# Optimization experiments

Measured on AMD Instinct MI355X. Metric: run time of the kernel, lower is better.

Reference implementation:

```python
import jax, jax.numpy as jnp
import numpy as np

M = 64    # multiplicity (channels per harmonic degree)
P = 64    # positional encoding dim
EPS = 1e-5


def sinusoidal_pe(N, P):
    pos = jnp.arange(N, dtype=jnp.float32)[:, None]
    div = jnp.exp(jnp.arange(0, P, 2, dtype=jnp.float32) * (-np.log(10000.0) / P))
    pe = jnp.zeros((N, P), dtype=jnp.float32)
    pe = pe.at[:, 0::2].set(jnp.sin(pos * div))
    pe = pe.at[:, 1::2].set(jnp.cos(pos * div))
    return pe


def split_irreps(h):
    # h: [B, N, 4M] -> scalar part [B,N,M], vector part [B,N,M,3]
    B, N, _ = h.shape
    h4 = h.reshape(B, N, M, 4)
    return h4[..., 0], h4[..., 1:]


def merge_irreps(s, v):
    B, N, _ = s.shape
    return jnp.concatenate([s[..., None], v], axis=-1).reshape(B, N, M * 4)


def hyena_block(h, Wq, Wk, Wv, filt, Wo):
    # Hyena-style gated long convolution: q * conv(k * v), FFT circular conv along seq
    N = h.shape[1]
    q = h @ Wq
    k = h @ Wk
    v = h @ Wv
    kf = jnp.fft.rfft(filt, n=N, axis=0)                       # [N//2+1, H]
    conv = jnp.fft.irfft(jnp.fft.rfft(k * v, n=N, axis=1) * kf[None], n=N, axis=1)
    return (q * conv) @ Wo


def reg_linear(h, W0, W1):
    # degree-wise linear mixing across multiplicity (equivariant)
    s, v = split_irreps(h)
    return merge_irreps(jnp.einsum('bnm,mk->bnk', s, W0),
                        jnp.einsum('bnmd,mk->bnkd', v, W1))


def reg_batchnorm(h, g0, g1):
    # normalize per-channel irrep norms over (batch, tokens); learnable per-channel gain
    s, v = split_irreps(h)
    n0 = jnp.sqrt(jnp.mean(s * s, axis=(0, 1)) + EPS)          # [M]
    n1 = jnp.sqrt(jnp.mean(jnp.sum(v * v, axis=-1), axis=(0, 1)) + EPS)
    return merge_irreps(s / n0 * g0, v / n1[:, None] * g1[:, None])


def norm_activation(h):
    # norm-gated nonlinearity: each irrep scaled by sigmoid of its norm (equivariant)
    s, v = split_irreps(h)
    vn = jnp.sqrt(jnp.sum(v * v, axis=-1, keepdims=True) + EPS)
    return merge_irreps(s * jax.nn.sigmoid(jnp.abs(s)), v * jax.nn.sigmoid(vn))


def setup_inputs() -> dict:
    key = jax.random.key(0)
    B, N = 64, 1024
    D = M * 4
    H = [360, 360, 160]   # 10*sum(2l+1,l<=5)=360, 360, 10*sum(2l+1,l<=3)=160
    ks = iter(jax.random.split(key, 64))
    def rn(shape, scale=0.02):
        return jax.random.normal(next(ks), shape, dtype=jnp.float32) * scale
    inp = {
        'x': jax.random.normal(next(ks), (B, N, 3), dtype=jnp.float32),
        'tok_emb': rn((3, P)),
        'Wf': rn((P, M)),
        'wv': rn((M,), 0.5),
        'w_out': rn((M,), 0.5),
    }
    for i, Hi in enumerate(H, start=1):
        inp[f'Wq{i}'] = rn((D, Hi)); inp[f'Wk{i}'] = rn((D, Hi)); inp[f'Wv{i}'] = rn((D, Hi))
        inp[f'filt{i}'] = rn((N, Hi)); inp[f'Wo{i}'] = rn((Hi, D))
        inp[f'Wm0_{i}'] = rn((M, M)); inp[f'Wm1_{i}'] = rn((M, M))
        inp[f'g0_{i}'] = jnp.ones((M,), jnp.float32); inp[f'g1_{i}'] = jnp.ones((M,), jnp.float32)
    return inp


def reference(x, tok_emb, Wf, wv, w_out,
              Wq1, Wk1, Wv1, filt1, Wo1, Wm0_1, Wm1_1, g0_1, g1_1,
              Wq2, Wk2, Wv2, filt2, Wo2, Wm0_2, Wm1_2, g0_2, g1_2,
              Wq3, Wk3, Wv3, filt3, Wo3, Wm0_3, Wm1_3, g0_3, g1_3):
    B, N, _ = x.shape
    # invariant features: sinusoidal PE + token-type embedding (alternating 0/1, last token 2)
    pe = sinusoidal_pe(N, P)
    tt = jnp.arange(N) % 2
    tt = tt.at[-1].set(2)
    f = pe + tok_emb[tt]                                        # [N, P]
    # input conversion: invariants -> degree-0 channels; input vector -> degree-1 channels
    s0 = jnp.broadcast_to((f @ Wf)[None], (B, N, M))
    v0 = x[:, :, None, :] * wv[None, None, :, None]             # [B, N, M, 3]
    h = merge_irreps(s0, v0)                                    # [B, N, 4M]
    layers = [
        (Wq1, Wk1, Wv1, filt1, Wo1, Wm0_1, Wm1_1, g0_1, g1_1),
        (Wq2, Wk2, Wv2, filt2, Wo2, Wm0_2, Wm1_2, g0_2, g1_2),
        (Wq3, Wk3, Wv3, filt3, Wo3, Wm0_3, Wm1_3, g0_3, g1_3),
    ]
    for (Wq, Wk, Wv_, filt, Wo, Wm0, Wm1, g0, g1) in layers:
        h = h + hyena_block(h, Wq, Wk, Wv_, filt, Wo)           # hyena + residual
        y = reg_linear(h, Wm0, Wm1)                             # mlp
        y = reg_batchnorm(y, g0, g1)                            # batch norm
        y = norm_activation(y)                                  # norm activation
        h = h + y                                               # residual
    pooled = h.mean(axis=1)                                     # [B, 4M] mean pool over tokens
    _, vpool = split_irreps(pooled[:, None, :])                 # [B, 1, M, 3]
    return jnp.einsum('bmd,m->bd', vpool[:, 0], w_out)          # [B, 3]
```

## Files before the change

### kernel.cpp

```cpp
#include <hip/hip_runtime.h>
#include <math.h>

namespace {

typedef __bf16 bf16_t;
typedef bf16_t bf16x8 __attribute__((ext_vector_type(8)));
typedef float floatx4 __attribute__((ext_vector_type(4)));

constexpr int kN = 1024;
constexpr int kM = 64;
constexpr int kP = 64;
constexpr float kEps = 1e-5f;
constexpr int kFN = 1024;
constexpr size_t kYOFF = 16777216;

__device__ __forceinline__ float sigmoidf(float v) { return 1.0f / (1.0f + expf(-v)); }

__device__ __forceinline__ floatx4 mfma16(bf16x8 a, bf16x8 b, floatx4 c) {
  return __builtin_amdgcn_mfma_f32_16x16x32_bf16(a, b, c, 0, 0, 0);
}

__device__ __forceinline__ void fma3(floatx4& acc, bf16x8 ah, bf16x8 al,
                                     bf16x8 bh, bf16x8 bl) {
  acc = mfma16(ah, bh, acc);
  acc = mfma16(ah, bl, acc);
  acc = mfma16(al, bh, acc);
}

__device__ __forceinline__ void fma2(floatx4& acc, bf16x8 ah, bf16x8 bh, bf16x8 bl) {
  acc = mfma16(ah, bh, acc);
  acc = mfma16(ah, bl, acc);
}

union U4 { uint4 u; bf16_t b[8]; };
union Pk4 { uint2 u; bf16_t b[4]; };
union Ub2 { uint u; bf16_t b[2]; };

__device__ __forceinline__ void glds16(const bf16_t* g, bf16_t* l) {
  __builtin_amdgcn_global_load_lds(
      (const __attribute__((address_space(1))) void*)g,
      (__attribute__((address_space(3))) void*)l, 16, 0, 0);
}

__device__ __forceinline__ size_t hidx(int r, int d8) {
  const int rb = r >> 6, rr = r & 63;
  return (size_t)(rb * 8 + (d8 >> 2)) * 4096 + (rr >> 4) * 1024 + (d8 & 3) * 128 + (rr & 15) * 8;
}

__device__ __forceinline__ int zi(int i) { return i + (i >> 4); }

__device__ __forceinline__ float2 cadd(float2 a, float2 b) { return {a.x + b.x, a.y + b.y}; }
__device__ __forceinline__ float2 csub(float2 a, float2 b) { return {a.x - b.x, a.y - b.y}; }
__device__ __forceinline__ float2 cmul(float2 a, float2 w) {
  return {a.x * w.x - a.y * w.y, a.x * w.y + a.y * w.x};
}
__device__ __forceinline__ float2 cmulc(float2 a, float2 w) {
  return {a.x * w.x + a.y * w.y, a.y * w.x - a.x * w.y};
}

__global__ void k_s0(const float* __restrict__ tok_emb, const float* __restrict__ Wf,
                     float* __restrict__ s0) {
  __shared__ float f[kP];
  const int n = blockIdx.x;
  const int t = threadIdx.x;
  const int tt = (n == kN - 1) ? 2 : (n & 1);
  const int j = t >> 1;
  const float cexp = (float)(-9.210340371976184 / 64.0);
  const float divj = expf((float)(2 * j) * cexp);
  const float ang = (float)n * divj;
  const float pe = (t & 1) ? cosf(ang) : sinf(ang);
  f[t] = pe + tok_emb[tt * kP + t];
  __syncthreads();
  float acc = 0.0f;
#pragma unroll 8
  for (int p = 0; p < kP; ++p) acc = fmaf(f[p], Wf[p * kM + t], acc);
  s0[n * kM + t] = acc;
}

__global__ void k_h0(const float* __restrict__ x, const float* __restrict__ wv,
                     const float* __restrict__ s0, bf16_t* __restrict__ hsh) {
  const int idx = blockIdx.x * 256 + threadIdx.x;
  const int r = idx >> 5, d8 = idx & 31;
  const int n = r & (kN - 1);
  const int m0 = d8 * 2, m1 = m0 + 1;
  const float w0 = wv[m0], w1 = wv[m1];
  const float x0 = x[r * 3 + 0], x1 = x[r * 3 + 1], x2 = x[r * 3 + 2];
  float f[8];
  f[0] = s0[n * kM + m0]; f[1] = x0 * w0; f[2] = x1 * w0; f[3] = x2 * w0;
  f[4] = s0[n * kM + m1]; f[5] = x0 * w1; f[6] = x1 * w1; f[7] = x2 * w1;
  U4 oh, ol;
#pragma unroll
  for (int i = 0; i < 8; ++i) {
    const bf16_t h_ = (bf16_t)f[i];
    oh.b[i] = h_; ol.b[i] = (bf16_t)(f[i] - (float)h_);
  }
  const size_t base = hidx(r, d8);
  *(uint4*)(hsh + base) = oh.u;
  *(uint4*)(hsh + base + 512) = ol.u;
}

__global__ void k_wqkv3(const float* __restrict__ Wq0, const float* __restrict__ Wk0,
                        const float* __restrict__ Wv0,
                        const float* __restrict__ Wq1, const float* __restrict__ Wk1,
                        const float* __restrict__ Wv1,
                        const float* __restrict__ Wq2, const float* __restrict__ Wk2,
                        const float* __restrict__ Wv2, bf16_t* __restrict__ wall3) {
  const int l = blockIdx.y;
  const int H = (l == 2) ? 160 : 360;
  const int gy = (l == 2) ? 3 : 6;
  const int c = blockIdx.x;
  if (c >= gy * 64) return;
  const int k = threadIdx.x;
  const float* Wq = (l == 0) ? Wq0 : ((l == 1) ? Wq1 : Wq2);
  const float* Wk = (l == 0) ? Wk0 : ((l == 1) ? Wk1 : Wk2);
  const float* Wv = (l == 0) ? Wv0 : ((l == 1) ? Wv1 : Wv2);
  bf16_t* wall = wall3 + ((l == 2) ? 1179648 : (size_t)l * 589824);
  const bool ok = c < H;
  const float w[3] = {ok ? Wq[k * H + c] : 0.f, ok ? Wk[k * H + c] : 0.f,
                      ok ? Wv[k * H + c] : 0.f};
  const int ct = c >> 6, cgrp = (c >> 4) & 3, cl = c & 15;
  const int kc = k >> 5, quad = (k >> 3) & 3, off = k & 7;
  const size_t base = (size_t)(ct * 8 + kc) * 12288 + cgrp * 512 + quad * 128 + cl * 8 + off;
#pragma unroll
  for (int mat = 0; mat < 3; ++mat) {
    const bf16_t hi = (bf16_t)w[mat];
    wall[base + mat * 4096] = hi;
    wall[base + mat * 4096 + 2048] = (bf16_t)(w[mat] - (float)hi);
  }
}

__global__ void k_wo3(const float* __restrict__ Wo0, const float* __restrict__ Wo1,
                      const float* __restrict__ Wo2, bf16_t* __restrict__ WoF3) {
  const int l = blockIdx.y;
  const int H = (l == 2) ? 160 : 360;
  const float* Wo = (l == 0) ? Wo0 : ((l == 1) ? Wo1 : Wo2);
  bf16_t* WoF = WoF3 + (size_t)l * 196608;
  const int d = blockIdx.x;
  const int c = threadIdx.x;
  const float w = (c < H) ? Wo[c * 256 + d] : 0.f;
  const int dt = d >> 6, dgrp = (d >> 4) & 3, dl = d & 15;
  const int kc = c >> 5, quad = (c >> 3) & 3, off = c & 7;
  const size_t base = (size_t)(dt * 12 + kc) * 4096 + dgrp * 512 + quad * 128 + dl * 8 + off;
  const bf16_t hi = (bf16_t)w;
  WoF[base] = hi;
  WoF[base + 2048] = (bf16_t)(w - (float)hi);
}

__global__ void k_bt3(const float* __restrict__ W00, const float* __restrict__ W10,
                      const float* __restrict__ W01, const float* __restrict__ W11,
                      const float* __restrict__ W02, const float* __restrict__ W12,
                      bf16_t* __restrict__ BtF3) {
  const int l = blockIdx.y;
  const float* W0 = (l == 0) ? W00 : ((l == 1) ? W01 : W02);
  const float* W1 = (l == 0) ? W10 : ((l == 1) ? W11 : W12);
  bf16_t* BtF = BtF3 + (size_t)l * 131072;
  const int col = blockIdx.x, row = threadIdx.x;
  const int k = col >> 2, ck = col & 3, m = row >> 2, cm = row & 3;
  float v = 0.f;
  if (cm == ck) v = (ck == 0 ? W0 : W1)[m * 64 + k];
  const int ct = col >> 6, cgrp = (col >> 4) & 3, cl = col & 15;
  const int kc = row >> 5, quad = (row >> 3) & 3, off = row & 7;
  const size_t base = (size_t)(ct * 8 + kc) * 4096 + cgrp * 512 + quad * 128 + cl * 8 + off;
  const bf16_t hi = (bf16_t)v;
  BtF[base] = hi;
  BtF[base + 2048] = (bf16_t)(v - (float)hi);
}

__global__ void k_tw(float2* __restrict__ twg) {
  const int j = blockIdx.x * 256 + threadIdx.x;
  if (j < kFN / 2) {
    float s, c;
    sincosf(-6.283185307179586f * (float)j / (float)kFN, &s, &c);
    twg[j].x = c; twg[j].y = s;
  }
}

__device__ __forceinline__ void dif_step(float2* z, const float2* tw, int m, int p) {
  const int pm = p & (m - 1);
  const int j = ((p & ~(m - 1)) << 2) | pm;
  const int tm2 = 512 / (2 * m), tm1 = 512 / m;
  const float2 x0 = z[zi(j)], x1 = z[zi(j + m)];
  const float2 x2 = z[zi(j + 2 * m)], x3 = z[zi(j + 3 * m)];
  const float2 w2 = tw[pm * tm2], w2b = tw[(pm + m) * tm2], w1 = tw[pm * tm1];
  const float2 a0 = cadd(x0, x2), a2 = cmul(csub(x0, x2), w2);
  const float2 a1 = cadd(x1, x3), a3 = cmul(csub(x1, x3), w2b);
  z[zi(j)]         = cadd(a0, a1);
  z[zi(j + m)]     = cmul(csub(a0, a1), w1);
  z[zi(j + 2 * m)] = cadd(a2, a3);
  z[zi(j + 3 * m)] = cmul(csub(a2, a3), w1);
}

__device__ __forceinline__ void dit_step(float2* z, const float2* tw, int m, int p) {
  const int pm = p & (m - 1);
  const int j = ((p & ~(m - 1)) << 2) | pm;
  const int tm2 = 512 / (2 * m), tm1 = 512 / m;
  const float2 x0 = z[zi(j)], x1 = z[zi(j + m)];
  const float2 x2 = z[zi(j + 2 * m)], x3 = z[zi(j + 3 * m)];
  const float2 w1 = tw[pm * tm1], w2 = tw[pm * tm2], w2b = tw[(pm + m) * tm2];
  const float2 c1 = cmulc(x1, w1), c3 = cmulc(x3, w1);
  const float2 b0 = cadd(x0, c1), b1 = csub(x0, c1);
  const float2 b2 = cadd(x2, c3), b3 = csub(x2, c3);
  const float2 d2 = cmulc(b2, w2), d3 = cmulc(b3, w2b);
  z[zi(j)]         = cadd(b0, d2);
  z[zi(j + 2 * m)] = csub(b0, d2);
  z[zi(j + m)]     = cadd(b1, d3);
  z[zi(j + 3 * m)] = csub(b1, d3);
}

__device__ void fft_dif(float2* z, const float2* tw) {
  const int p = threadIdx.x;
#pragma unroll
  for (int m = 256; m >= 1; m >>= 2) {
    __syncthreads();
    dif_step(z, tw, m, p);
  }
}

__device__ void fft_dif2(float2* za, float2* zb, const float2* tw) {
  const int p = threadIdx.x;
#pragma unroll
  for (int m = 256; m >= 1; m >>= 2) {
    __syncthreads();
    dif_step(za, tw, m, p);
    dif_step(zb, tw, m, p);
  }
}

__device__ void fft_dit_inv2(float2* za, float2* zb, const float2* tw) {
  const int p = threadIdx.x;
#pragma unroll
  for (int m = 1; m <= 256; m <<= 2) {
    __syncthreads();
    dit_step(za, tw, m, p);
    dit_step(zb, tw, m, p);
  }
}

__global__ __launch_bounds__(256) void k_kf3(const float* __restrict__ f0,
    const float* __restrict__ f1, const float* __restrict__ f2,
    const float2* __restrict__ twg, float2* __restrict__ kf3) {
  __shared__ float2 z[kFN + kFN / 16];
  __shared__ float2 tw[kFN / 2];
  const int bid = blockIdx.x;
  const int l = (bid < 360) ? 0 : ((bid < 720) ? 1 : 2);
  const int c = bid - ((l == 0) ? 0 : ((l == 1) ? 360 : 720));
  const int H = (l == 2) ? 160 : 360;
  const float* filt = (l == 0) ? f0 : ((l == 1) ? f1 : f2);
  float2* kf = kf3 + (size_t)l * 368640;
  for (int j = threadIdx.x; j < kFN / 2; j += 256) tw[j] = twg[j];
  for (int n = threadIdx.x; n < kFN; n += 256) {
    z[zi(n)].x = filt[n * H + c];
    z[zi(n)].y = 0.0f;
  }
  fft_dif(z, tw);
  __syncthreads();
  for (int j = threadIdx.x; j < kFN; j += 256) kf[c * kFN + j] = z[zi(j)];
}

__global__ __launch_bounds__(256) void k_conv(const bf16_t* __restrict__ kvb,
    const bf16_t* __restrict__ qb, bf16_t* __restrict__ prodb,
    const float2* __restrict__ kf, const float2* __restrict__ twg, int H) {
  __shared__ float2 za[kFN + kFN / 16];
  __shared__ float2 zb[kFN + kFN / 16];
  __shared__ float2 tw[kFN / 2];
  const int blk = blockIdx.x;
  const int c = blk % H;
  const int pb = blk / H;
  const size_t off0 = ((size_t)((4 * pb) * H + c)) << 10;
  const size_t off1 = ((size_t)((4 * pb + 1) * H + c)) << 10;
  const size_t off2 = ((size_t)((4 * pb + 2) * H + c)) << 10;
  const size_t off3 = ((size_t)((4 * pb + 3) * H + c)) << 10;
  for (int j = threadIdx.x; j < kFN / 2; j += 256) tw[j] = twg[j];
  for (int n2 = threadIdx.x; n2 < 512; n2 += 256) {
    Ub2 a0, a1, a2, a3;
    a0.u = *(const uint*)(kvb + off0 + 2 * n2);
    a1.u = *(const uint*)(kvb + off1 + 2 * n2);
    a2.u = *(const uint*)(kvb + off2 + 2 * n2);
    a3.u = *(const uint*)(kvb + off3 + 2 * n2);
    za[zi(2 * n2)].x = (float)a0.b[0];     za[zi(2 * n2)].y = (float)a1.b[0];
    za[zi(2 * n2 + 1)].x = (float)a0.b[1]; za[zi(2 * n2 + 1)].y = (float)a1.b[1];
    zb[zi(2 * n2)].x = (float)a2.b[0];     zb[zi(2 * n2)].y = (float)a3.b[0];
    zb[zi(2 * n2 + 1)].x = (float)a2.b[1]; zb[zi(2 * n2 + 1)].y = (float)a3.b[1];
  }
  fft_dif2(za, zb, tw);
  __syncthreads();
  for (int j = threadIdx.x; j < kFN; j += 256) {
    const float2 b = kf[c * kFN + j];
    const float2 a = za[zi(j)];
    float2 o;
    o.x = a.x * b.x - a.y * b.y;
    o.y = a.x * b.y + a.y * b.x;
    za[zi(j)] = o;
    const float2 a2_ = zb[zi(j)];
    float2 o2;
    o2.x = a2_.x * b.x - a2_.y * b.y;
    o2.y = a2_.x * b.y + a2_.y * b.x;
    zb[zi(j)] = o2;
  }
  fft_dit_inv2(za, zb, tw);
  __syncthreads();
  const float s = 1.0f / (float)kFN;
  for (int n2 = threadIdx.x; n2 < 512; n2 += 256) {
    Ub2 q0, q1, q2, q3, o0, o1, o2, o3;
    q0.u = *(const uint*)(qb + off0 + 2 * n2);
    q1.u = *(const uint*)(qb + off1 + 2 * n2);
    q2.u = *(const uint*)(qb + off2 + 2 * n2);
    q3.u = *(const uint*)(qb + off3 + 2 * n2);
    o0.b[0] = (bf16_t)((za[zi(2 * n2)].x * s) * (float)q0.b[0]);
    o0.b[1] = (bf16_t)((za[zi(2 * n2 + 1)].x * s) * (float)q0.b[1]);
    o1.b[0] = (bf16_t)((za[zi(2 * n2)].y * s) * (float)q1.b[0]);
    o1.b[1] = (bf16_t)((za[zi(2 * n2 + 1)].y * s) * (float)q1.b[1]);
    o2.b[0] = (bf16_t)((zb[zi(2 * n2)].x * s) * (float)q2.b[0]);
    o2.b[1] = (bf16_t)((zb[zi(2 * n2 + 1)].x * s) * (float)q2.b[1]);
    o3.b[0] = (bf16_t)((zb[zi(2 * n2)].y * s) * (float)q3.b[0]);
    o3.b[1] = (bf16_t)((zb[zi(2 * n2 + 1)].y * s) * (float)q3.b[1]);
    *(uint*)(prodb + off0 + 2 * n2) = o0.u;
    *(uint*)(prodb + off1 + 2 * n2) = o1.u;
    *(uint*)(prodb + off2 + 2 * n2) = o2.u;
    *(uint*)(prodb + off3 + 2 * n2) = o3.u;
  }
}

__global__ __launch_bounds__(256) void k_qkv(const bf16_t* __restrict__ hsh,
    const bf16_t* __restrict__ wall, int H,
    bf16_t* __restrict__ qtb, bf16_t* __restrict__ kvb) {
  __shared__ bf16_t lds[20480];
  const int gy = (H + 63) >> 6;
  const int bid = blockIdx.x;
  const int xcd = bid & 7, sseq = bid >> 3;
  const int ct = sseq % gy;
  const int rb2 = (sseq / gy) * 8 + xcd;
  const int rb0 = rb2 * 2, rb1 = rb0 + 1;
  const int t = threadIdx.x;
  const int lane = t & 63, wave = t >> 6;
  const int l15 = lane & 15, quad = lane >> 4;
  const int c0 = ct * 64;
  const int wr = (wave & 1) * 32, wc = (wave >> 1) * 32;
  const int wr16 = (wave & 1) * 2, wc16 = (wave >> 1) * 2;
  const int q128l = quad * 128 + l15 * 8;
  floatx4 aq[2][2][2] = {}, ak_[2][2][2] = {}, av_[2][2][2] = {};
  for (int kt = 0; kt < 8; ++kt) {
    {
      const bf16_t* A0 = hsh + (size_t)(rb0 * 8 + kt) * 4096;
      const bf16_t* A1 = hsh + (size_t)(rb1 * 8 + kt) * 4096;
      const bf16_t* Bs = wall + (size_t)(ct * 8 + kt) * 12288;
#pragma unroll
      for (int s = 0; s < 10; ++s) {
        const int seg = wave * 10 + s;
        const bf16_t* src = (seg < 8) ? (A0 + seg * 512)
                          : (seg < 16) ? (A1 + (seg - 8) * 512)
                                       : (Bs + (seg - 16) * 512);
        glds16(src + lane * 8, &lds[seg * 512]);
      }
    }
    __syncthreads();
    bf16x8 ah[2][2], al[2][2];
#pragma unroll
    for (int rbx = 0; rbx < 2; ++rbx)
#pragma unroll
      for (int i = 0; i < 2; ++i) {
        ah[rbx][i] = *(const bf16x8*)(lds + rbx * 4096 + ((wr16 + i) * 2 + 0) * 512 + q128l);
        al[rbx][i] = *(const bf16x8*)(lds + rbx * 4096 + ((wr16 + i) * 2 + 1) * 512 + q128l);
      }
#pragma unroll
    for (int mat = 0; mat < 3; ++mat) {
      const int bb = 8192 + mat * 4096;
#pragma unroll
      for (int j = 0; j < 2; ++j) {
        const bf16x8 bh = *(const bf16x8*)(lds + bb + (wc16 + j) * 512 + q128l);
        const bf16x8 bl = *(const bf16x8*)(lds + bb + 2048 + (wc16 + j) * 512 + q128l);
#pragma unroll
        for (int rbx = 0; rbx < 2; ++rbx)
#pragma unroll
          for (int i = 0; i < 2; ++i) {
            floatx4& a = (mat == 0) ? aq[rbx][i][j]
                       : (mat == 1) ? ak_[rbx][i][j] : av_[rbx][i][j];
            fma3(a, ah[rbx][i], al[rbx][i], bh, bl);
          }
      }
    }
    __syncthreads();
  }
#pragma unroll
  for (int rbx = 0; rbx < 2; ++rbx) {
    const int r0 = (rb0 + rbx) * 64;
    const int b = r0 >> 10;
    const int n0 = r0 & 1023;
#pragma unroll
    for (int j = 0; j < 2; ++j) {
      const int c = c0 + wc + j * 16 + l15;
      if (c < H) {
        const size_t rbw = (((size_t)(b * H + c)) << 10) + n0 + wr + quad * 4;
#pragma unroll
        for (int i = 0; i < 2; ++i) {
          Pk4 pq, pk;
#pragma unroll
          for (int r = 0; r < 4; ++r) {
            pq.b[r] = (bf16_t)aq[rbx][i][j][r];
            pk.b[r] = (bf16_t)(ak_[rbx][i][j][r] * av_[rbx][i][j][r]);
          }
          *(uint2*)(qtb + rbw + i * 16) = pq.u;
          *(uint2*)(kvb + rbw + i * 16) = pk.u;
        }
      }
    }
  }
}

__global__ __launch_bounds__(256) void k_mix(const bf16_t* __restrict__ pv, int H, int KT,
    const bf16_t* __restrict__ WoF, bf16_t* __restrict__ hsh) {
  __shared__ float smem[4352];
  bf16_t* lsm = (bf16_t*)smem;
  const int r0 = blockIdx.x * 64;
  const int t = threadIdx.x;
  const int lane = t & 63, wave = t >> 6;
  const int l15 = lane & 15, quad = lane >> 4;
  const int b = r0 >> 10, n0 = r0 & 1023;
  const int wr = (wave & 1) * 32, wh = wave >> 1;
  const int q128l = quad * 128 + l15 * 8;
  floatx4 acc[2][8] = {};
  const int cl = t >> 3, n8 = (t & 7) * 8;
  for (int kt = 0; kt < KT; ++kt) {
    const int ck0 = kt * 32;
    __syncthreads();
    {
      const int c = ck0 + cl;
      U4 val;
      val.u = make_uint4(0, 0, 0, 0);
      if (c < H)
        val.u = *(const uint4*)(pv + ((((size_t)(b * H + c)) << 10) + n0 + n8));
#pragma unroll
      for (int u = 0; u < 8; ++u) lsm[(n8 + u) * 40 + cl] = val.b[u];
    }
    __syncthreads();
    const bf16x8 ah0 = *(const bf16x8*)(lsm + (wr + l15) * 40 + quad * 8);
    const bf16x8 ah1 = *(const bf16x8*)(lsm + (wr + 16 + l15) * 40 + quad * 8);
#pragma unroll
    for (int j = 0; j < 8; ++j) {
      const int jj = wh * 8 + j;
      const int dt = jj >> 2, dgrp = jj & 3;
      const bf16_t* Bb = WoF + (size_t)(dt * 12 + kt) * 4096 + dgrp * 512 + q128l;
      const bf16x8 bh = *(const bf16x8*)Bb;
      const bf16x8 bl = *(const bf16x8*)(Bb + 2048);
      fma2(acc[0][j], ah0, bh, bl);
      fma2(acc[1][j], ah1, bh, bl);
    }
  }
  const int nl = t >> 2, q4 = t & 3;
  const int r = r0 + nl;
#pragma unroll
  for (int g = 0; g < 4; ++g) {
    __syncthreads();
    if (wh == (g >> 1)) {
#pragma unroll
      for (int jl = 0; jl < 4; ++jl) {
        const int j = (g & 1) * 4 + jl;
#pragma unroll
        for (int i = 0; i < 2; ++i)
#pragma unroll
          for (int rr = 0; rr < 4; ++rr)
            smem[(wr + i * 16 + quad * 4 + rr) * 68 + jl * 16 + l15] = acc[i][j][rr];
      }
    }
    __syncthreads();
#pragma unroll
    for (int u8 = 0; u8 < 2; ++u8) {
      const int d8 = g * 8 + q4 * 2 + u8;
      const size_t base = hidx(r, d8);
      U4 hi, lo;
      hi.u = *(const uint4*)(hsh + base);
      lo.u = *(const uint4*)(hsh + base + 512);
      U4 oh, ol;
#pragma unroll
      for (int i = 0; i < 8; ++i) {
        const float f = (float)hi.b[i] + (float)lo.b[i] +
                        smem[nl * 68 + (q4 * 2 + u8) * 8 + i];
        const bf16_t h_ = (bf16_t)f;
        oh.b[i] = h_; ol.b[i] = (bf16_t)(f - (float)h_);
      }
      *(uint4*)(hsh + base) = oh.u;
      *(uint4*)(hsh + base + 512) = ol.u;
    }
  }
}

__global__ __launch_bounds__(256) void k_reg(const bf16_t* __restrict__ hsh,
    const bf16_t* __restrict__ BtF,
    bf16_t* __restrict__ ybf, float* __restrict__ partial) {
  __shared__ float smf[12288];
  __shared__ float red[256];
  bf16_t* lds = (bf16_t*)smf;
  const int bid = blockIdx.x;
  const int xcd = bid & 7, sseq = bid >> 3;
  const int ct = sseq & 3;
  const int rb2 = (sseq >> 2) * 8 + xcd;
  const int rb0 = rb2 * 2, rb1 = rb0 + 1;
  const int t = threadIdx.x;
  const int lane = t & 63, wave = t >> 6;
  const int l15 = lane & 15, quad = lane >> 4;
  const int c0 = ct * 64;
  const int wr = (wave & 1) * 32, wc = (wave >> 1) * 32;
  const int wr16 = (wave & 1) * 2, wc16 = (wave >> 1) * 2;
  const int q128l = quad * 128 + l15 * 8;
  floatx4 acc[2][2][2] = {};
  auto stage = [&](int kt, int buf) {
    const bf16_t* A0 = hsh + (size_t)(rb0 * 8 + kt) * 4096;
    const bf16_t* A1 = hsh + (size_t)(rb1 * 8 + kt) * 4096;
    const bf16_t* Bs = BtF + (size_t)(ct * 8 + kt) * 4096;
#pragma unroll
    for (int s = 0; s < 6; ++s) {
      const int seg = wave * 6 + s;
      const bf16_t* src = (seg < 8) ? (A0 + seg * 512)
                        : (seg < 16) ? (A1 + (seg - 8) * 512)
                                     : (Bs + (seg - 16) * 512);
      glds16(src + lane * 8, &lds[buf * 12288 + seg * 512]);
    }
  };
  stage(0, 0);
  __syncthreads();
  for (int kt = 0; kt < 8; ++kt) {
    const int cur = kt & 1;
    if (kt < 7) stage(kt + 1, cur ^ 1);
    const bf16_t* Lb = lds + cur * 12288;
    bf16x8 ah[2][2], al[2][2];
#pragma unroll
    for (int rbx = 0; rbx < 2; ++rbx)
#pragma unroll
      for (int i = 0; i < 2; ++i) {
        ah[rbx][i] = *(const bf16x8*)(Lb + rbx * 4096 + ((wr16 + i) * 2 + 0) * 512 + q128l);
        al[rbx][i] = *(const bf16x8*)(Lb + rbx * 4096 + ((wr16 + i) * 2 + 1) * 512 + q128l);
      }
#pragma unroll
    for (int j = 0; j < 2; ++j) {
      const bf16x8 bh = *(const bf16x8*)(Lb + 8192 + (wc16 + j) * 512 + q128l);
      const bf16x8 bl = *(const bf16x8*)(Lb + 8192 + 2048 + (wc16 + j) * 512 + q128l);
#pragma unroll
      for (int rbx = 0; rbx < 2; ++rbx)
#pragma unroll
        for (int i = 0; i < 2; ++i)
          fma3(acc[rbx][i][j], ah[rbx][i], al[rbx][i], bh, bl);
    }
    __syncthreads();
  }
#pragma unroll
  for (int rbx = 0; rbx < 2; ++rbx)
#pragma unroll
    for (int j = 0; j < 2; ++j) {
      float s = 0.f;
#pragma unroll
      for (int i = 0; i < 2; ++i)
#pragma unroll
        for (int r = 0; r < 4; ++r)
          s = fmaf(acc[rbx][i][j][r], acc[rbx][i][j][r], s);
      s += __shfl_down(s, 32);
      s += __shfl_down(s, 16);
      if (lane < 16) red[rbx * 128 + wave * 32 + j * 16 + lane] = s;
    }
#pragma unroll
  for (int rbx = 0; rbx < 2; ++rbx) {
    __syncthreads();
#pragma unroll
    for (int i = 0; i < 2; ++i)
#pragma unroll
      for (int j = 0; j < 2; ++j)
#pragma unroll
        for (int r = 0; r < 4; ++r)
          smf[(wr + i * 16 + quad * 4 + r) * 68 + wc + j * 16 + l15] = acc[rbx][i][j][r];
    __syncthreads();
    const int nl = t >> 2, q4 = t & 3;
    const int r0 = (rb0 + rbx) * 64;
    const size_t gi = (size_t)(r0 + nl) * 256 + c0 + q4 * 16;
#pragma unroll
    for (int u2 = 0; u2 < 2; ++u2) {
      U4 oh, ol;
#pragma unroll
      for (int i = 0; i < 8; ++i) {
        const float f = smf[nl * 68 + q4 * 16 + u2 * 8 + i];
        const bf16_t h_ = (bf16_t)f;
        oh.b[i] = h_; ol.b[i] = (bf16_t)(f - (float)h_);
      }
      *(uint4*)(ybf + gi + u2 * 8) = oh.u;
      *(uint4*)(ybf + kYOFF + gi + u2 * 8) = ol.u;
    }
  }
  if (t < 64) {
    const int w0 = (t >= 32) ? 2 : 0;
    const float v0 = red[w0 * 32 + (t & 31)] + red[(w0 + 1) * 32 + (t & 31)];
    const float v1 = red[128 + w0 * 32 + (t & 31)] + red[128 + (w0 + 1) * 32 + (t & 31)];
    partial[(size_t)rb0 * 256 + c0 + t] = v0;
    partial[(size_t)rb1 * 256 + c0 + t] = v1;
  }
}

__global__ __launch_bounds__(256) void k_stat(const float* __restrict__ partial,
                                              float* __restrict__ st) {
  __shared__ float sm1[16][16];
  __shared__ float tot[16];
  const int bb = blockIdx.x;
  const int t = threadIdx.x;
  const int col16 = t & 15, rgrp = t >> 4;
  const int c = bb * 16 + col16;
  float s = 0.f;
  for (int r = rgrp; r < 1024; r += 16) s += partial[(size_t)r * 256 + c];
  sm1[rgrp][col16] = s;
  __syncthreads();
  if (t < 16) {
    float v = 0.f;
#pragma unroll
    for (int g = 0; g < 16; ++g) v += sm1[g][t];
    tot[t] = v;
  }
  __syncthreads();
  if (t < 4) {
    const int m = bb * 4 + t;
    st[m] = tot[4 * t];
    st[64 + m] = tot[4 * t + 1] + tot[4 * t + 2] + tot[4 * t + 3];
  }
}

__global__ void k_bnact(const bf16_t* __restrict__ ybf, const float* __restrict__ stats,
    const float* __restrict__ g0, const float* __restrict__ g1, bf16_t* __restrict__ hsh) {
  const int idx = blockIdx.x * 256 + threadIdx.x;
  const int r = idx >> 5, d8 = idx & 31;
  const int m0 = d8 * 2, m1 = m0 + 1;
  const float i00 = g0[m0] / sqrtf(stats[m0] * (1.0f / 65536.0f) + kEps);
  const float i10 = g1[m0] / sqrtf(stats[64 + m0] * (1.0f / 65536.0f) + kEps);
  const float i01 = g0[m1] / sqrtf(stats[m1] * (1.0f / 65536.0f) + kEps);
  const float i11 = g1[m1] / sqrtf(stats[64 + m1] * (1.0f / 65536.0f) + kEps);
  const size_t ye = (size_t)r * 256 + d8 * 8;
  U4 yh, yl;
  yh.u = *(const uint4*)(ybf + ye);
  yl.u = *(const uint4*)(ybf + kYOFF + ye);
  float yv[8];
#pragma unroll
  for (int i = 0; i < 8; ++i) yv[i] = (float)yh.b[i] + (float)yl.b[i];
  float a[8];
  {
    const float s = yv[0] * i00;
    const float vx = yv[1] * i10, vy = yv[2] * i10, vz = yv[3] * i10;
    const float so = s * sigmoidf(fabsf(s));
    const float vn = sqrtf(fmaf(vx, vx, fmaf(vy, vy, vz * vz)) + kEps);
    const float gv = sigmoidf(vn);
    a[0] = so; a[1] = vx * gv; a[2] = vy * gv; a[3] = vz * gv;
  }
  {
    const float s = yv[4] * i01;
    const float vx = yv[5] * i11, vy = yv[6] * i11, vz = yv[7] * i11;
    const float so = s * sigmoidf(fabsf(s));
    const float vn = sqrtf(fmaf(vx, vx, fmaf(vy, vy, vz * vz)) + kEps);
    const float gv = sigmoidf(vn);
    a[4] = so; a[5] = vx * gv; a[6] = vy * gv; a[7] = vz * gv;
  }
  const size_t base = hidx(r, d8);
  U4 hi, lo;
  hi.u = *(const uint4*)(hsh + base);
  lo.u = *(const uint4*)(hsh + base + 512);
  U4 oh, ol;
#pragma unroll
  for (int i = 0; i < 8; ++i) {
    const float f = (float)hi.b[i] + (float)lo.b[i] + a[i];
    const bf16_t h_ = (bf16_t)f;
    oh.b[i] = h_; ol.b[i] = (bf16_t)(f - (float)h_);
  }
  *(uint4*)(hsh + base) = oh.u;
  *(uint4*)(hsh + base + 512) = ol.u;
}

__global__ __launch_bounds__(256) void k_pool(const bf16_t* __restrict__ hsh,
    const float* __restrict__ w_out, float* __restrict__ out) {
  __shared__ float r0s[256], r1s[256], r2s[256];
  const int b = blockIdx.x;
  const int t = threadIdx.x;
  float p0 = 0, p1 = 0, p2 = 0;
  for (int idx = t; idx < kN * 32; idx += 256) {
    const int n = idx >> 5, d8 = idx & 31;
    const int r = (b << 10) + n;
    const size_t base = hidx(r, d8);
    U4 hi, lo;
    hi.u = *(const uint4*)(hsh + base);
    lo.u = *(const uint4*)(hsh + base + 512);
    const float w0 = w_out[d8 * 2], w1 = w_out[d8 * 2 + 1];
    p0 += ((float)hi.b[1] + (float)lo.b[1]) * w0 + ((float)hi.b[5] + (float)lo.b[5]) * w1;
    p1 += ((float)hi.b[2] + (float)lo.b[2]) * w0 + ((float)hi.b[6] + (float)lo.b[6]) * w1;
    p2 += ((float)hi.b[3] + (float)lo.b[3]) * w0 + ((float)hi.b[7] + (float)lo.b[7]) * w1;
  }
  r0s[t] = p0; r1s[t] = p1; r2s[t] = p2;
  __syncthreads();
  for (int s = 128; s > 0; s >>= 1) {
    if (t < s) { r0s[t] += r0s[t + s]; r1s[t] += r1s[t + s]; r2s[t] += r2s[t + s]; }
    __syncthreads();
  }
  if (t == 0) {
    out[b * 3 + 0] = r0s[0] * (1.0f / kN);
    out[b * 3 + 1] = r1s[0] * (1.0f / kN);
    out[b * 3 + 2] = r2s[0] * (1.0f / kN);
  }
}

}

extern "C" void kernel_launch(void* const* d_in, const int* in_sizes, int n_in,
                              void* d_out, int out_size, void* d_ws, size_t ws_size,
                              hipStream_t stream) {
  const float* x       = (const float*)d_in[0];
  const float* tok_emb = (const float*)d_in[1];
  const float* Wf      = (const float*)d_in[2];
  const float* wv      = (const float*)d_in[3];
  const float* w_out   = (const float*)d_in[4];

  float* ws    = (float*)d_ws;
  bf16_t* hsh  = (bf16_t*)ws;
  bf16_t* kvb  = (bf16_t*)(ws + 16777216);
  bf16_t* qtb  = (bf16_t*)(ws + 28573696);
  bf16_t* prodb = (bf16_t*)(ws + 40370176);
  bf16_t* ybf  = prodb;
  float*  partial = ws + 40370176 + 20000000;
  float*  s0   = ws + 40370176 + 23592960;
  float*  kf3  = s0 + 65536;
  bf16_t* wall3 = (bf16_t*)(kf3 + 1802240);
  bf16_t* WoF3  = wall3 + 1474560;
  bf16_t* BtF3  = WoF3 + 589824;
  float* stats = (float*)(BtF3 + 393216);
  float* twg   = stats + 384;

  k_tw<<<2, 256, 0, stream>>>((float2*)twg);
  k_s0<<<kN, 64, 0, stream>>>(tok_emb, Wf, s0);
  k_h0<<<8192, 256, 0, stream>>>(x, wv, s0, hsh);
  k_wqkv3<<<dim3(384, 3), 256, 0, stream>>>(
      (const float*)d_in[5], (const float*)d_in[6], (const float*)d_in[7],
      (const float*)d_in[14], (const float*)d_in[15], (const float*)d_in[16],
      (const float*)d_in[23], (const float*)d_in[24], (const float*)d_in[25], wall3);
  k_wo3<<<dim3(256, 3), 384, 0, stream>>>(
      (const float*)d_in[9], (const float*)d_in[18], (const float*)d_in[27], WoF3);
  k_bt3<<<dim3(256, 3), 256, 0, stream>>>(
      (const float*)d_in[10], (const float*)d_in[11],
      (const float*)d_in[19], (const float*)d_in[20],
      (const float*)d_in[28], (const float*)d_in[29], BtF3);
  k_kf3<<<880, 256, 0, stream>>>(
      (const float*)d_in[8], (const float*)d_in[17], (const float*)d_in[26],
      (const float2*)twg, (float2*)kf3);

  for (int l = 0; l < 3; ++l) {
    const float* g0   = (const float*)d_in[5 + 9 * l + 7];
    const float* g1   = (const float*)d_in[5 + 9 * l + 8];
    const int H = (l == 2) ? 160 : 360;
    const int gy = (H + 63) / 64;
    const int KT = gy * 2;
    bf16_t* wall = wall3 + ((l == 2) ? 1179648 : (size_t)l * 589824);
    bf16_t* WoF  = WoF3 + (size_t)l * 196608;
    bf16_t* BtF  = BtF3 + (size_t)l * 131072;
    const float2* kf = (const float2*)kf3 + (size_t)l * 368640;
    float* st = stats + l * 128;

    k_qkv<<<gy * 512, 256, 0, stream>>>(hsh, wall, H, qtb, kvb);
    k_conv<<<16 * H, 256, 0, stream>>>(kvb, qtb, prodb, kf, (const float2*)twg, H);
    k_mix<<<1024, 256, 0, stream>>>(prodb, H, KT, WoF, hsh);
    k_reg<<<2048, 256, 0, stream>>>(hsh, BtF, ybf, partial);
    k_stat<<<16, 256, 0, stream>>>(partial, st);
    k_bnact<<<8192, 256, 0, stream>>>(ybf, st, g0, g1, hsh);
  }

  k_pool<<<64, 256, 0, stream>>>(hsh, w_out, (float*)d_out);
}
```

Baseline: 1.146 ms.

## Fuse last FFT radix-4 stages with spectral multiply; double-buffer k_mix LDS loads

The final DIF radix-4 stage, the pointwise multiply by the filter spectrum, and the first inverse DIT stage are merged into one register-resident pass per thread. This removes two barrier-separated shared-memory sweeps from the FFT convolution kernel. Separately, k_mix now prefetches the next K-tile from global memory into registers and writes it to a second LDS buffer, dropping one barrier per iteration and overlapping loads with MFMA work. The fused stage assumes each thread owns four consecutive bins, and the double buffer uses 2×2560 bf16 of the existing shared array.

```diff
diff --git a/kernel.cpp b/kernel.cpp
--- a/kernel.cpp
+++ b/kernel.cpp
@@ -216,20 +216,20 @@
   }
 }
 
-__device__ void fft_dif2(float2* za, float2* zb, const float2* tw) {
+__device__ void fft_dif2_hi(float2* za, float2* zb, const float2* tw) {
   const int p = threadIdx.x;
 #pragma unroll
-  for (int m = 256; m >= 1; m >>= 2) {
+  for (int m = 256; m >= 4; m >>= 2) {
     __syncthreads();
     dif_step(za, tw, m, p);
     dif_step(zb, tw, m, p);
   }
 }
 
-__device__ void fft_dit_inv2(float2* za, float2* zb, const float2* tw) {
+__device__ void fft_dit_inv2_hi(float2* za, float2* zb, const float2* tw) {
   const int p = threadIdx.x;
 #pragma unroll
-  for (int m = 1; m <= 256; m <<= 2) {
+  for (int m = 4; m <= 256; m <<= 2) {
     __syncthreads();
     dit_step(za, tw, m, p);
     dit_step(zb, tw, m, p);
@@ -282,22 +282,36 @@
     zb[zi(2 * n2)].x = (float)a2.b[0];     zb[zi(2 * n2)].y = (float)a3.b[0];
     zb[zi(2 * n2 + 1)].x = (float)a2.b[1]; zb[zi(2 * n2 + 1)].y = (float)a3.b[1];
   }
-  fft_dif2(za, zb, tw);
+  fft_dif2_hi(za, zb, tw);
   __syncthreads();
-  for (int j = threadIdx.x; j < kFN; j += 256) {
-    const float2 b = kf[c * kFN + j];
-    const float2 a = za[zi(j)];
-    float2 o;
-    o.x = a.x * b.x - a.y * b.y;
-    o.y = a.x * b.y + a.y * b.x;
-    za[zi(j)] = o;
-    const float2 a2_ = zb[zi(j)];
-    float2 o2;
-    o2.x = a2_.x * b.x - a2_.y * b.y;
-    o2.y = a2_.x * b.y + a2_.y * b.x;
-    zb[zi(j)] = o2;
-  }
-  fft_dit_inv2(za, zb, tw);
+  {
+    const int p = threadIdx.x;
+    const float2 B0 = kf[c * kFN + 4 * p + 0];
+    const float2 B1 = kf[c * kFN + 4 * p + 1];
+    const float2 B2 = kf[c * kFN + 4 * p + 2];
+    const float2 B3 = kf[c * kFN + 4 * p + 3];
+#pragma unroll
+    for (int arr = 0; arr < 2; ++arr) {
+      float2* z = arr ? zb : za;
+      const float2 x0 = z[zi(4 * p)], x1 = z[zi(4 * p + 1)];
+      const float2 x2 = z[zi(4 * p + 2)], x3 = z[zi(4 * p + 3)];
+      const float2 a0 = cadd(x0, x2), a2 = csub(x0, x2);
+      const float2 a1 = cadd(x1, x3), dd = csub(x1, x3);
+      const float2 a3 = {dd.y, -dd.x};
+      const float2 y0 = cadd(a0, a1), y1 = csub(a0, a1);
+      const float2 y2 = cadd(a2, a3), y3 = csub(a2, a3);
+      const float2 o0 = cmul(y0, B0), o1 = cmul(y1, B1);
+      const float2 o2 = cmul(y2, B2), o3 = cmul(y3, B3);
+      const float2 t0 = cadd(o0, o1), t1 = csub(o0, o1);
+      const float2 t2 = cadd(o2, o3), t3 = csub(o2, o3);
+      const float2 d3 = {-t3.y, t3.x};
+      z[zi(4 * p)]     = cadd(t0, t2);
+      z[zi(4 * p + 2)] = csub(t0, t2);
+      z[zi(4 * p + 1)] = cadd(t1, d3);
+      z[zi(4 * p + 3)] = csub(t1, d3);
+    }
+  }
+  fft_dit_inv2_hi(za, zb, tw);
   __syncthreads();
   const float s = 1.0f / (float)kFN;
   for (int n2 = threadIdx.x; n2 < 512; n2 += 256) {
@@ -420,21 +434,28 @@
   const int q128l = quad * 128 + l15 * 8;
   floatx4 acc[2][8] = {};
   const int cl = t >> 3, n8 = (t & 7) * 8;
+  {
+    U4 val;
+    val.u = make_uint4(0, 0, 0, 0);
+    if (cl < H)
+      val.u = *(const uint4*)(pv + ((((size_t)(b * H + cl)) << 10) + n0 + n8));
+#pragma unroll
+    for (int u = 0; u < 8; ++u) lsm[(n8 + u) * 40 + cl] = val.b[u];
+  }
   for (int kt = 0; kt < KT; ++kt) {
-    const int ck0 = kt * 32;
-    __syncthreads();
-    {
-      const int c = ck0 + cl;
-      U4 val;
-      val.u = make_uint4(0, 0, 0, 0);
+    const int cur = kt & 1;
+    const bool have = (kt + 1 < KT);
+    U4 nxt;
+    nxt.u = make_uint4(0, 0, 0, 0);
+    if (have) {
+      const int c = (kt + 1) * 32 + cl;
       if (c < H)
-        val.u = *(const uint4*)(pv + ((((size_t)(b * H + c)) << 10) + n0 + n8));
-#pragma unroll
-      for (int u = 0; u < 8; ++u) lsm[(n8 + u) * 40 + cl] = val.b[u];
-    }
-    __syncthreads();
-    const bf16x8 ah0 = *(const bf16x8*)(lsm + (wr + l15) * 40 + quad * 8);
-    const bf16x8 ah1 = *(const bf16x8*)(lsm + (wr + 16 + l15) * 40 + quad * 8);
+        nxt.u = *(const uint4*)(pv + ((((size_t)(b * H + c)) << 10) + n0 + n8));
+    }
+    __syncthreads();
+    const bf16_t* Ls = lsm + cur * 2560;
+    const bf16x8 ah0 = *(const bf16x8*)(Ls + (wr + l15) * 40 + quad * 8);
+    const bf16x8 ah1 = *(const bf16x8*)(Ls + (wr + 16 + l15) * 40 + quad * 8);
 #pragma unroll
     for (int j = 0; j < 8; ++j) {
       const int jj = wh * 8 + j;
@@ -444,6 +465,11 @@
       const bf16x8 bl = *(const bf16x8*)(Bb + 2048);
       fma2(acc[0][j], ah0, bh, bl);
       fma2(acc[1][j], ah1, bh, bl);
+    }
+    if (have) {
+      bf16_t* Ld = lsm + (cur ^ 1) * 2560;
+#pragma unroll
+      for (int u = 0; u < 8; ++u) Ld[(n8 + u) * 40 + cl] = nxt.b[u];
     }
   }
   const int nl = t >> 2, q4 = t & 3;
```

New measurement: 1.120 ms. -2.2%, faster.
